# Kernel optimization log

Measured on AMD Instinct MI355X. Metric: run time of the kernel, lower is better.

Reference implementation:

```python
import jax, jax.numpy as jnp
import numpy as np

NEG = -1e10

def setup_inputs() -> dict:
    key = jax.random.key(0)
    ks = jax.random.split(key, 7)
    B, Q, K = 8, 128, 512
    d_q, d_kv, d_attn = 512, 512, 256
    query = jax.random.normal(ks[0], (B, Q, d_q), dtype=jnp.float32)
    kv = jax.random.normal(ks[1], (B, K, d_kv), dtype=jnp.float32)
    query_len = jax.random.randint(ks[2], (B,), 1, Q + 1)
    kv_len = jax.random.randint(ks[3], (B,), 1, K + 1)
    # h2attn: Linear(d_q+d_kv, d_attn) -> weight [d_attn, d_q+d_kv], bias [d_attn]
    W = jax.random.normal(ks[4], (d_attn, d_q + d_kv), dtype=jnp.float32) / np.sqrt(d_q + d_kv)
    b = jnp.zeros((d_attn,), dtype=jnp.float32)
    v = jax.random.normal(ks[5], (d_attn,), dtype=jnp.float32)
    return {"query": query, "kv": kv, "W": W, "b": b, "v": v,
            "query_len": query_len, "kv_len": kv_len}

def reference(query, kv, W, b, v, query_len, kv_len):
    B, Q, d_q = query.shape
    _, K, d_kv = kv.shape
    # Split the concat-linear: W @ [q; kv] == Wq @ q + Wk @ kv (same math, no huge concat)
    Wq, Wk = W[:, :d_q], W[:, d_q:]
    q_proj = jnp.einsum('bqd,ad->bqa', query, Wq)   # [B,Q,d_attn]
    k_proj = jnp.einsum('bkd,ad->bka', kv, Wk)      # [B,K,d_attn]
    e = jnp.tanh(q_proj[:, :, None, :] + k_proj[:, None, :, :] + b)  # [B,Q,K,d_attn]
    score = jnp.einsum('bqka,a->bqk', e, v)          # [B,Q,K]
    mask_q = jnp.arange(Q)[None, :] < query_len[:, None]   # [B,Q]
    mask_k = jnp.arange(K)[None, :] < kv_len[:, None]      # [B,K]
    score = jnp.where(mask_q[:, :, None], score, NEG)
    score = jnp.where(mask_k[:, None, :], score, NEG)
    attn = jax.nn.softmax(score, axis=-1)
    out = jnp.einsum('bqk,bkd->bqd', attn, kv)       # [B,Q,d_kv]
    return out
```

## Files before the change

kernel.cpp:

```cpp
#include <hip/hip_runtime.h>

#define NEGV (-10000000000.0f)

typedef unsigned short u16;
typedef _Float16 __attribute__((ext_vector_type(8))) f16x8;
typedef _Float16 __attribute__((ext_vector_type(4))) f16x4;
typedef __attribute__((ext_vector_type(4))) float f32x4;

__device__ __forceinline__ u16 f2fh(float f) {
  _Float16 h = (_Float16)f;
  return __builtin_bit_cast(u16, h);
}

__device__ __forceinline__ void gload16(const u16* g, u16* l) {
  __builtin_amdgcn_global_load_lds(
      (const __attribute__((address_space(1))) void*)g,
      (__attribute__((address_space(3))) void*)l, 16, 0, 0);
}

__device__ __forceinline__ f16x8 cvt8(float4 x, float4 y) {
  f16x8 o;
  o[0] = (_Float16)x.x; o[1] = (_Float16)x.y;
  o[2] = (_Float16)x.z; o[3] = (_Float16)x.w;
  o[4] = (_Float16)y.x; o[5] = (_Float16)y.y;
  o[6] = (_Float16)y.z; o[7] = (_Float16)y.w;
  return o;
}

__device__ __forceinline__ void mfma_tile(const u16* sA, const u16* sB,
                                          int l, int wr, int wc,
                                          f32x4 (*acc)[2]) {
#pragma unroll
  for (int ks = 0; ks < 2; ks++) {
    f16x8 af[2], bfr[2];
#pragma unroll
    for (int f = 0; f < 2; f++) {
      int cb = (ks * 32 + ((l >> 4) << 3)) << 1;
      int row = wr * 32 + f * 16 + (l & 15);
      af[f] = *(const f16x8*)((const char*)sA + row * 128 + (cb ^ ((row & 7) << 4)));
      int col = wc * 32 + f * 16 + (l & 15);
      bfr[f] = *(const f16x8*)((const char*)sB + col * 128 + (cb ^ ((col & 7) << 4)));
    }
#pragma unroll
    for (int fm = 0; fm < 2; fm++)
#pragma unroll
      for (int fn = 0; fn < 2; fn++)
        acc[fm][fn] = __builtin_amdgcn_mfma_f32_16x16x32_f16(
            af[fm], bfr[fn], acc[fm][fn], 0, 0, 0);
  }
}

__global__ __launch_bounds__(256) void proj_mfma(
    const float* __restrict__ query, const float* __restrict__ kv,
    const float* __restrict__ W, const float* __restrict__ bias,
    float* __restrict__ qpE, float* __restrict__ kpE)
{
  __shared__ __align__(16) u16 sA[8 * 512];
  __shared__ __align__(16) u16 sB[8 * 512];
  const int id = blockIdx.x, t = threadIdx.x;

  const float *A, *B; float* C;
  int lda, ldb, ldc, bm, bn;
  const float* bp = nullptr;
  if (id < 64) {
    A = query; lda = 512; B = W; ldb = 1024;
    C = qpE; ldc = 256;
    bm = (id >> 2) * 64; bn = (id & 3) * 64;
    bp = bias;
  } else {
    int r = id - 64;
    int b = r >> 5, w5 = r & 31;
    A = W + 512; lda = 1024;
    B = kv + (size_t)b * 512 * 512; ldb = 512;
    C = kpE + (size_t)b * 256 * 512; ldc = 512;
    bm = (w5 & 3) * 64; bn = (w5 >> 2) * 64;
  }

  const int l = t & 63, w = t >> 6;
  const int wr = w >> 1, wc = w & 1;
  const int r0 = t >> 3, oc = t & 7;
  const int sw0 = (oc * 16) ^ ((r0 & 7) << 4);

  f32x4 acc[2][2] = {};
  float4 a00, a01, a10, a11, b00, b01, b10, b11;

  auto LOAD = [&](int k0) {
    const float* pa0 = A + (size_t)(bm + r0) * lda + k0 + oc * 8;
    const float* pa1 = pa0 + (size_t)32 * lda;
    a00 = *(const float4*)pa0; a01 = *(const float4*)(pa0 + 4);
    a10 = *(const float4*)pa1; a11 = *(const float4*)(pa1 + 4);
    const float* pb0 = B + (size_t)(bn + r0) * ldb + k0 + oc * 8;
    const float* pb1 = pb0 + (size_t)32 * ldb;
    b00 = *(const float4*)pb0; b01 = *(const float4*)(pb0 + 4);
    b10 = *(const float4*)pb1; b11 = *(const float4*)(pb1 + 4);
  };
  auto WRITE = [&]() {
    *(f16x8*)((char*)sA + r0 * 128 + sw0)        = cvt8(a00, a01);
    *(f16x8*)((char*)sA + (r0 + 32) * 128 + sw0) = cvt8(a10, a11);
    *(f16x8*)((char*)sB + r0 * 128 + sw0)        = cvt8(b00, b01);
    *(f16x8*)((char*)sB + (r0 + 32) * 128 + sw0) = cvt8(b10, b11);
  };

  LOAD(0);
  for (int k0 = 0; k0 < 512; k0 += 64) {
    __syncthreads();
    WRITE();
    if (k0 + 64 < 512) LOAD(k0 + 64);
    __syncthreads();
    mfma_tile(sA, sB, l, wr, wc, acc);
  }

#pragma unroll
  for (int fm = 0; fm < 2; fm++)
#pragma unroll
    for (int fn = 0; fn < 2; fn++) {
      int cn = bn + wc * 32 + fn * 16 + (l & 15);
      float bv = bp ? bp[cn] : 0.0f;
#pragma unroll
      for (int j = 0; j < 4; j++) {
        int rm = bm + wr * 32 + fm * 16 + (l >> 4) * 4 + j;
        C[(size_t)rm * ldc + cn] = __expf((acc[fm][fn][j] + bv) * 2.0f);
      }
    }
}

__global__ __launch_bounds__(256) void score_softmax(
    const float* __restrict__ qpE,
    const float* __restrict__ kpE,
    const float* __restrict__ v,
    const int* __restrict__ qlen_p, const int* __restrict__ klen_p,
    u16* __restrict__ P)
{
  const int b = blockIdx.y, q0 = blockIdx.x * 2, t = threadIdx.x;
  const int qlen = qlen_p[b], klen = klen_p[b];
  const int w = t >> 6, l = t & 63;
  const int k1 = w * 64 + l, k2 = k1 + 256;
  u16* Pb = P + (size_t)(b * 128 + q0) * 512;

  if (q0 >= qlen) {
    const u16 uh = f2fh(1.0f / 512.0f);
    Pb[k1] = uh; Pb[k2] = uh;
    Pb[512 + k1] = uh; Pb[512 + k2] = uh;
    return;
  }

  __shared__ float sEq[512];
  __shared__ float sV2[256];
  __shared__ float sRed[16];

  sV2[t] = 2.0f * v[t];
  sEq[t]       = qpE[(size_t)(b * 128 + q0) * 256 + t];
  sEq[256 + t] = qpE[(size_t)(b * 128 + q0 + 1) * 256 + t];
  __syncthreads();

  const float* kc = kpE + (size_t)b * 256 * 512;
  float s1a = 0.f, s2a = 0.f, s1b = 0.f, s2b = 0.f;

  if (w * 64 < klen) {
    if (256 + w * 64 < klen) {
#pragma unroll 8
      for (int a = 0; a < 256; a++) {
        float ek1 = kc[(size_t)a * 512 + k1];
        float ek2 = kc[(size_t)a * 512 + k2];
        float vv = sV2[a];
        float eqA = sEq[a], eqB = sEq[256 + a];
        s1a = fmaf(-vv, __builtin_amdgcn_rcpf(fmaf(eqA, ek1, 1.0f)), s1a);
        s2a = fmaf(-vv, __builtin_amdgcn_rcpf(fmaf(eqA, ek2, 1.0f)), s2a);
        s1b = fmaf(-vv, __builtin_amdgcn_rcpf(fmaf(eqB, ek1, 1.0f)), s1b);
        s2b = fmaf(-vv, __builtin_amdgcn_rcpf(fmaf(eqB, ek2, 1.0f)), s2b);
      }
    } else {
#pragma unroll 8
      for (int a = 0; a < 256; a++) {
        float ek1 = kc[(size_t)a * 512 + k1];
        float vv = sV2[a];
        float eqA = sEq[a], eqB = sEq[256 + a];
        s1a = fmaf(-vv, __builtin_amdgcn_rcpf(fmaf(eqA, ek1, 1.0f)), s1a);
        s1b = fmaf(-vv, __builtin_amdgcn_rcpf(fmaf(eqB, ek1, 1.0f)), s1b);
      }
    }
  }

  if (k1 >= klen) { s1a = NEGV; s1b = NEGV; }
  if (k2 >= klen) { s2a = NEGV; s2b = NEGV; }

  float mA = fmaxf(s1a, s2a), mB = fmaxf(s1b, s2b);
#pragma unroll
  for (int off = 32; off > 0; off >>= 1) {
    mA = fmaxf(mA, __shfl_xor(mA, off));
    mB = fmaxf(mB, __shfl_xor(mB, off));
  }
  if (l == 0) { sRed[w * 4 + 0] = mA; sRed[w * 4 + 1] = mB; }
  __syncthreads();
  const float MA = fmaxf(fmaxf(sRed[0], sRed[4]), fmaxf(sRed[8],  sRed[12]));
  const float MB = fmaxf(fmaxf(sRed[1], sRed[5]), fmaxf(sRed[9],  sRed[13]));

  float e1a = __expf(s1a - MA), e2a = __expf(s2a - MA);
  float e1b = __expf(s1b - MB), e2b = __expf(s2b - MB);
  float suA = e1a + e2a, suB = e1b + e2b;
#pragma unroll
  for (int off = 32; off > 0; off >>= 1) {
    suA += __shfl_xor(suA, off);
    suB += __shfl_xor(suB, off);
  }
  if (l == 0) { sRed[w * 4 + 2] = suA; sRed[w * 4 + 3] = suB; }
  __syncthreads();
  const float SA = (sRed[2] + sRed[6]) + (sRed[10] + sRed[14]);
  const float SB = (sRed[3] + sRed[7]) + (sRed[11] + sRed[15]);
  const float rA = __fdividef(1.0f, SA);
  const float rB = __fdividef(1.0f, SB);

  Pb[k1] = f2fh(e1a * rA);
  Pb[k2] = f2fh(e2a * rA);
  if (q0 + 1 < qlen) {
    Pb[512 + k1] = f2fh(e1b * rB);
    Pb[512 + k2] = f2fh(e2b * rB);
  } else {
    const u16 uh = f2fh(1.0f / 512.0f);
    Pb[512 + k1] = uh;
    Pb[512 + k2] = uh;
  }
}

__global__ __launch_bounds__(256) void pv_mfma(
    const u16* __restrict__ P, const float* __restrict__ kv,
    float* __restrict__ out)
{
  __shared__ __align__(16) u16 sA[8 * 512];
  __shared__ __align__(16) u16 sB[8 * 512];
  const int id = blockIdx.x, t = threadIdx.x;
  const int b = id >> 4, r = id & 15;
  const int bm = (r >> 3) * 64, bn = (r & 7) * 64;

  const u16* Ab = P + (size_t)b * 128 * 512;
  const float* Bb = kv + (size_t)b * 512 * 512;

  const int l = t & 63, w = t >> 6;
  const int wr = w >> 1, wc = w & 1;
  const int srow = l >> 3, scol = ((l & 7) ^ srow) << 3;

  const int dq = t & 15, kq = t >> 4;

  float4 v0, v1, v2, v3;
  auto LOADB = [&](int k0) {
    const float* p = Bb + (size_t)(k0 + kq * 4) * 512 + bn + dq * 4;
    v0 = *(const float4*)p;
    v1 = *(const float4*)(p + 512);
    v2 = *(const float4*)(p + 1024);
    v3 = *(const float4*)(p + 1536);
  };
  auto WRITEB = [&]() {
#define WRB(jj, ee)                                                       \
    { int d = dq * 4 + jj;                                                \
      f16x4 c; c[0] = (_Float16)v0.ee; c[1] = (_Float16)v1.ee;            \
      c[2] = (_Float16)v2.ee; c[3] = (_Float16)v3.ee;                     \
      *(f16x4*)((char*)sB + d * 128 +                                     \
                ((((kq >> 1) * 16) ^ ((d & 7) << 4)) + (kq & 1) * 8)) = c; }
    WRB(0, x) WRB(1, y) WRB(2, z) WRB(3, w)
#undef WRB
  };

  f32x4 acc[2][2] = {};
  LOADB(0);
  for (int k0 = 0; k0 < 512; k0 += 64) {
    __syncthreads();
    WRITEB();
#pragma unroll
    for (int i = 0; i < 2; i++) {
      int s = w * 2 + i;
      gload16(Ab + (size_t)(bm + s * 8 + srow) * 512 + k0 + scol, sA + s * 512);
    }
    if (k0 + 64 < 512) LOADB(k0 + 64);
    __syncthreads();
    mfma_tile(sA, sB, l, wr, wc, acc);
  }

  float* Cb = out + (size_t)b * 128 * 512;
#pragma unroll
  for (int fm = 0; fm < 2; fm++)
#pragma unroll
    for (int fn = 0; fn < 2; fn++) {
      int cn = bn + wc * 32 + fn * 16 + (l & 15);
#pragma unroll
      for (int j = 0; j < 4; j++) {
        int rm = bm + wr * 32 + fm * 16 + (l >> 4) * 4 + j;
        Cb[(size_t)rm * 512 + cn] = acc[fm][fn][j];
      }
    }
}

extern "C" void kernel_launch(void* const* d_in, const int* in_sizes, int n_in,
                              void* d_out, int out_size, void* d_ws, size_t ws_size,
                              hipStream_t stream)
{
  const float* query = (const float*)d_in[0];
  const float* kv    = (const float*)d_in[1];
  const float* W     = (const float*)d_in[2];
  const float* bbias = (const float*)d_in[3];
  const float* v     = (const float*)d_in[4];
  const int*   qlen  = (const int*)d_in[5];
  const int*   klen  = (const int*)d_in[6];
  float* out = (float*)d_out;

  float* qpE = (float*)d_ws;
  float* kpE = qpE + 1024 * 256;
  u16*   P   = (u16*)(kpE + 8 * 256 * 512);

  proj_mfma<<<dim3(320), 256, 0, stream>>>(query, kv, W, bbias, qpE, kpE);

  score_softmax<<<dim3(64, 8), 256, 0, stream>>>(
      qpE, kpE, v, qlen, klen, P);

  pv_mfma<<<dim3(128), 256, 0, stream>>>(P, kv, out);
}
```

Baseline: 44.65 us.

## Fuse score softmax with PV product and precompute kv column sums

Merges the score/softmax kernel and the MFMA PV kernel into one kernel. Each block handles four queries, keeps the probabilities in LDS, and does P·V with FP32 FMAs over only the valid keys (up to klen), so the fp16 P round-trip through global memory and one launch go away. Fully masked query rows now take the mean of kv, computed once by extra column-sum blocks in the projection kernel using atomics, with a memset added to zero that buffer. The cost is that PV now runs on scalar FP32 instead of matrix cores, and the block is larger and uses a lot of LDS, which may limit occupancy.

```diff
diff --git a/kernel.cpp b/kernel.cpp
--- a/kernel.cpp
+++ b/kernel.cpp
@@ -4,19 +4,7 @@
 
 typedef unsigned short u16;
 typedef _Float16 __attribute__((ext_vector_type(8))) f16x8;
-typedef _Float16 __attribute__((ext_vector_type(4))) f16x4;
 typedef __attribute__((ext_vector_type(4))) float f32x4;
-
-__device__ __forceinline__ u16 f2fh(float f) {
-  _Float16 h = (_Float16)f;
-  return __builtin_bit_cast(u16, h);
-}
-
-__device__ __forceinline__ void gload16(const u16* g, u16* l) {
-  __builtin_amdgcn_global_load_lds(
-      (const __attribute__((address_space(1))) void*)g,
-      (__attribute__((address_space(3))) void*)l, 16, 0, 0);
-}
 
 __device__ __forceinline__ f16x8 cvt8(float4 x, float4 y) {
   f16x8 o;
@@ -50,14 +38,31 @@
   }
 }
 
-__global__ __launch_bounds__(256) void proj_mfma(
+__global__ __launch_bounds__(256) void proj_colsum(
     const float* __restrict__ query, const float* __restrict__ kv,
     const float* __restrict__ W, const float* __restrict__ bias,
-    float* __restrict__ qpE, float* __restrict__ kpE)
+    float* __restrict__ qpE, float* __restrict__ kpE,
+    float* __restrict__ kvsum)
 {
+  const int id = blockIdx.x, t = threadIdx.x;
+
+  if (id >= 320) {
+    const int cb = id - 320;
+    const int b = cb >> 3, kt = cb & 7;
+    const float* p = kv + ((size_t)b * 512 + kt * 64) * 512 + 2 * t;
+    float s0 = 0.f, s1 = 0.f;
+#pragma unroll 8
+    for (int kk = 0; kk < 64; kk++) {
+      float2 x = *(const float2*)(p + (size_t)kk * 512);
+      s0 += x.x; s1 += x.y;
+    }
+    atomicAdd(&kvsum[b * 512 + 2 * t], s0);
+    atomicAdd(&kvsum[b * 512 + 2 * t + 1], s1);
+    return;
+  }
+
   __shared__ __align__(16) u16 sA[8 * 512];
   __shared__ __align__(16) u16 sB[8 * 512];
-  const int id = blockIdx.x, t = threadIdx.x;
 
   const float *A, *B; float* C;
   int lda, ldb, ldc, bm, bn;
@@ -124,169 +129,141 @@
     }
 }
 
-__global__ __launch_bounds__(256) void score_softmax(
+__global__ __launch_bounds__(512) void score_pv(
     const float* __restrict__ qpE,
     const float* __restrict__ kpE,
     const float* __restrict__ v,
     const int* __restrict__ qlen_p, const int* __restrict__ klen_p,
-    u16* __restrict__ P)
-{
-  const int b = blockIdx.y, q0 = blockIdx.x * 2, t = threadIdx.x;
-  const int qlen = qlen_p[b], klen = klen_p[b];
-  const int w = t >> 6, l = t & 63;
-  const int k1 = w * 64 + l, k2 = k1 + 256;
-  u16* Pb = P + (size_t)(b * 128 + q0) * 512;
-
-  if (q0 >= qlen) {
-    const u16 uh = f2fh(1.0f / 512.0f);
-    Pb[k1] = uh; Pb[k2] = uh;
-    Pb[512 + k1] = uh; Pb[512 + k2] = uh;
-    return;
-  }
-
-  __shared__ float sEq[512];
-  __shared__ float sV2[256];
-  __shared__ float sRed[16];
-
-  sV2[t] = 2.0f * v[t];
-  sEq[t]       = qpE[(size_t)(b * 128 + q0) * 256 + t];
-  sEq[256 + t] = qpE[(size_t)(b * 128 + q0 + 1) * 256 + t];
-  __syncthreads();
-
-  const float* kc = kpE + (size_t)b * 256 * 512;
-  float s1a = 0.f, s2a = 0.f, s1b = 0.f, s2b = 0.f;
-
-  if (w * 64 < klen) {
-    if (256 + w * 64 < klen) {
-#pragma unroll 8
-      for (int a = 0; a < 256; a++) {
-        float ek1 = kc[(size_t)a * 512 + k1];
-        float ek2 = kc[(size_t)a * 512 + k2];
-        float vv = sV2[a];
-        float eqA = sEq[a], eqB = sEq[256 + a];
-        s1a = fmaf(-vv, __builtin_amdgcn_rcpf(fmaf(eqA, ek1, 1.0f)), s1a);
-        s2a = fmaf(-vv, __builtin_amdgcn_rcpf(fmaf(eqA, ek2, 1.0f)), s2a);
-        s1b = fmaf(-vv, __builtin_amdgcn_rcpf(fmaf(eqB, ek1, 1.0f)), s1b);
-        s2b = fmaf(-vv, __builtin_amdgcn_rcpf(fmaf(eqB, ek2, 1.0f)), s2b);
-      }
-    } else {
-#pragma unroll 8
-      for (int a = 0; a < 256; a++) {
-        float ek1 = kc[(size_t)a * 512 + k1];
-        float vv = sV2[a];
-        float eqA = sEq[a], eqB = sEq[256 + a];
-        s1a = fmaf(-vv, __builtin_amdgcn_rcpf(fmaf(eqA, ek1, 1.0f)), s1a);
-        s1b = fmaf(-vv, __builtin_amdgcn_rcpf(fmaf(eqB, ek1, 1.0f)), s1b);
-      }
-    }
-  }
-
-  if (k1 >= klen) { s1a = NEGV; s1b = NEGV; }
-  if (k2 >= klen) { s2a = NEGV; s2b = NEGV; }
-
-  float mA = fmaxf(s1a, s2a), mB = fmaxf(s1b, s2b);
-#pragma unroll
-  for (int off = 32; off > 0; off >>= 1) {
-    mA = fmaxf(mA, __shfl_xor(mA, off));
-    mB = fmaxf(mB, __shfl_xor(mB, off));
-  }
-  if (l == 0) { sRed[w * 4 + 0] = mA; sRed[w * 4 + 1] = mB; }
-  __syncthreads();
-  const float MA = fmaxf(fmaxf(sRed[0], sRed[4]), fmaxf(sRed[8],  sRed[12]));
-  const float MB = fmaxf(fmaxf(sRed[1], sRed[5]), fmaxf(sRed[9],  sRed[13]));
-
-  float e1a = __expf(s1a - MA), e2a = __expf(s2a - MA);
-  float e1b = __expf(s1b - MB), e2b = __expf(s2b - MB);
-  float suA = e1a + e2a, suB = e1b + e2b;
-#pragma unroll
-  for (int off = 32; off > 0; off >>= 1) {
-    suA += __shfl_xor(suA, off);
-    suB += __shfl_xor(suB, off);
-  }
-  if (l == 0) { sRed[w * 4 + 2] = suA; sRed[w * 4 + 3] = suB; }
-  __syncthreads();
-  const float SA = (sRed[2] + sRed[6]) + (sRed[10] + sRed[14]);
-  const float SB = (sRed[3] + sRed[7]) + (sRed[11] + sRed[15]);
-  const float rA = __fdividef(1.0f, SA);
-  const float rB = __fdividef(1.0f, SB);
-
-  Pb[k1] = f2fh(e1a * rA);
-  Pb[k2] = f2fh(e2a * rA);
-  if (q0 + 1 < qlen) {
-    Pb[512 + k1] = f2fh(e1b * rB);
-    Pb[512 + k2] = f2fh(e2b * rB);
-  } else {
-    const u16 uh = f2fh(1.0f / 512.0f);
-    Pb[512 + k1] = uh;
-    Pb[512 + k2] = uh;
-  }
-}
-
-__global__ __launch_bounds__(256) void pv_mfma(
-    const u16* __restrict__ P, const float* __restrict__ kv,
+    const float* __restrict__ kv,
+    const float* __restrict__ kvsum,
     float* __restrict__ out)
 {
-  __shared__ __align__(16) u16 sA[8 * 512];
-  __shared__ __align__(16) u16 sB[8 * 512];
-  const int id = blockIdx.x, t = threadIdx.x;
-  const int b = id >> 4, r = id & 15;
-  const int bm = (r >> 3) * 64, bn = (r & 7) * 64;
-
-  const u16* Ab = P + (size_t)b * 128 * 512;
-  const float* Bb = kv + (size_t)b * 512 * 512;
-
-  const int l = t & 63, w = t >> 6;
-  const int wr = w >> 1, wc = w & 1;
-  const int srow = l >> 3, scol = ((l & 7) ^ srow) << 3;
-
-  const int dq = t & 15, kq = t >> 4;
-
-  float4 v0, v1, v2, v3;
-  auto LOADB = [&](int k0) {
-    const float* p = Bb + (size_t)(k0 + kq * 4) * 512 + bn + dq * 4;
-    v0 = *(const float4*)p;
-    v1 = *(const float4*)(p + 512);
-    v2 = *(const float4*)(p + 1024);
-    v3 = *(const float4*)(p + 1536);
-  };
-  auto WRITEB = [&]() {
-#define WRB(jj, ee)                                                       \
-    { int d = dq * 4 + jj;                                                \
-      f16x4 c; c[0] = (_Float16)v0.ee; c[1] = (_Float16)v1.ee;            \
-      c[2] = (_Float16)v2.ee; c[3] = (_Float16)v3.ee;                     \
-      *(f16x4*)((char*)sB + d * 128 +                                     \
-                ((((kq >> 1) * 16) ^ ((d & 7) << 4)) + (kq & 1) * 8)) = c; }
-    WRB(0, x) WRB(1, y) WRB(2, z) WRB(3, w)
-#undef WRB
-  };
-
-  f32x4 acc[2][2] = {};
-  LOADB(0);
-  for (int k0 = 0; k0 < 512; k0 += 64) {
-    __syncthreads();
-    WRITEB();
-#pragma unroll
-    for (int i = 0; i < 2; i++) {
-      int s = w * 2 + i;
-      gload16(Ab + (size_t)(bm + s * 8 + srow) * 512 + k0 + scol, sA + s * 512);
-    }
-    if (k0 + 64 < 512) LOADB(k0 + 64);
-    __syncthreads();
-    mfma_tile(sA, sB, l, wr, wc, acc);
-  }
-
-  float* Cb = out + (size_t)b * 128 * 512;
-#pragma unroll
-  for (int fm = 0; fm < 2; fm++)
-#pragma unroll
-    for (int fn = 0; fn < 2; fn++) {
-      int cn = bn + wc * 32 + fn * 16 + (l & 15);
+  const int b = blockIdx.y, q0 = blockIdx.x * 4, t = threadIdx.x;
+  const int qlen = qlen_p[b], klen = klen_p[b];
+  float* outb = out + (size_t)(b * 128 + q0) * 512;
+
+  if (q0 >= qlen) {
+    float m = kvsum[b * 512 + t] * (1.0f / 512.0f);
+#pragma unroll
+    for (int r = 0; r < 4; r++) outb[(size_t)r * 512 + t] = m;
+    return;
+  }
+
+  __shared__ float sW[512][4];
+  __shared__ float sEq[256][4];
+  __shared__ float sV2[256];
+  __shared__ float sRed[8][8];
+  __shared__ float sAcc[4][4 * 512];
+
+  {
+    int a = t & 255, rr = t >> 8;
+    sEq[a][rr]     = qpE[(size_t)(b * 128 + q0 + rr) * 256 + a];
+    sEq[a][rr + 2] = qpE[(size_t)(b * 128 + q0 + rr + 2) * 256 + a];
+    if (t < 256) sV2[t] = 2.0f * v[t];
+  }
+  __syncthreads();
+
+  const int w = t >> 6, l = t & 63;
+  const int k = t;
+
+  float s[4] = {0.f, 0.f, 0.f, 0.f};
+  if (w * 64 < klen) {
+    const float* kc = kpE + (size_t)b * 256 * 512 + k;
+#pragma unroll 8
+    for (int a = 0; a < 256; a++) {
+      float ek = kc[(size_t)a * 512];
+      f32x4 eq = *(const f32x4*)&sEq[a][0];
+      float vv = sV2[a];
+#pragma unroll
+      for (int r = 0; r < 4; r++)
+        s[r] = fmaf(-vv, __builtin_amdgcn_rcpf(fmaf(eq[r], ek, 1.0f)), s[r]);
+    }
+  }
+  if (k >= klen) {
+#pragma unroll
+    for (int r = 0; r < 4; r++) s[r] = NEGV;
+  }
+
+#pragma unroll
+  for (int r = 0; r < 4; r++) {
+    float x = s[r];
+#pragma unroll
+    for (int off = 32; off > 0; off >>= 1) x = fmaxf(x, __shfl_xor(x, off));
+    if (l == 0) sRed[w][r] = x;
+  }
+  __syncthreads();
+  float e[4];
+#pragma unroll
+  for (int r = 0; r < 4; r++) {
+    float mm = sRed[0][r];
+#pragma unroll
+    for (int i = 1; i < 8; i++) mm = fmaxf(mm, sRed[i][r]);
+    e[r] = __expf(s[r] - mm);
+  }
+  __syncthreads();
+#pragma unroll
+  for (int r = 0; r < 4; r++) {
+    float x = e[r];
+#pragma unroll
+    for (int off = 32; off > 0; off >>= 1) x += __shfl_xor(x, off);
+    if (l == 0) sRed[w][4 + r] = x;
+  }
+  __syncthreads();
+  f32x4 p;
+#pragma unroll
+  for (int r = 0; r < 4; r++) {
+    float S = 0.f;
+#pragma unroll
+    for (int i = 0; i < 8; i++) S += sRed[i][4 + r];
+    p[r] = e[r] * __fdividef(1.0f, S);
+  }
+  *(f32x4*)&sW[k][0] = p;
+  __syncthreads();
+
+  f32x4 accA[4] = {}, accB[4] = {};
+  const int kb = w * 64;
+  const int ke = (kb + 64 < klen) ? kb + 64 : klen;
+  const float* kvb = kv + (size_t)b * 512 * 512 + l;
+#pragma unroll 4
+  for (int kk = kb; kk < ke; kk++) {
+    f32x4 p4 = *(const f32x4*)&sW[kk][0];
+    const float* row = kvb + (size_t)kk * 512;
+    float x[8];
+#pragma unroll
+    for (int j = 0; j < 8; j++) x[j] = row[j * 64];
+#pragma unroll
+    for (int r = 0; r < 4; r++)
 #pragma unroll
       for (int j = 0; j < 4; j++) {
-        int rm = bm + wr * 32 + fm * 16 + (l >> 4) * 4 + j;
-        Cb[(size_t)rm * 512 + cn] = acc[fm][fn][j];
+        accA[r][j] = fmaf(p4[r], x[j],     accA[r][j]);
+        accB[r][j] = fmaf(p4[r], x[4 + j], accB[r][j]);
       }
-    }
+  }
+
+  if (w < 4) {
+#pragma unroll
+    for (int r = 0; r < 4; r++)
+#pragma unroll
+      for (int j = 0; j < 8; j++)
+        sAcc[w][r * 512 + l + j * 64] = (j < 4) ? accA[r][j] : accB[r][j - 4];
+  }
+  __syncthreads();
+  if (w >= 4) {
+#pragma unroll
+    for (int r = 0; r < 4; r++)
+#pragma unroll
+      for (int j = 0; j < 8; j++)
+        sAcc[w - 4][r * 512 + l + j * 64] += (j < 4) ? accA[r][j] : accB[r][j - 4];
+  }
+  __syncthreads();
+
+#pragma unroll
+  for (int r = 0; r < 4; r++) {
+    float val = (sAcc[0][r * 512 + t] + sAcc[1][r * 512 + t]) +
+                (sAcc[2][r * 512 + t] + sAcc[3][r * 512 + t]);
+    if (q0 + r >= qlen) val = kvsum[b * 512 + t] * (1.0f / 512.0f);
+    outb[(size_t)r * 512 + t] = val;
+  }
 }
 
 extern "C" void kernel_launch(void* const* d_in, const int* in_sizes, int n_in,
@@ -302,14 +279,15 @@
   const int*   klen  = (const int*)d_in[6];
   float* out = (float*)d_out;
 
-  float* qpE = (float*)d_ws;
-  float* kpE = qpE + 1024 * 256;
-  u16*   P   = (u16*)(kpE + 8 * 256 * 512);
-
-  proj_mfma<<<dim3(320), 256, 0, stream>>>(query, kv, W, bbias, qpE, kpE);
-
-  score_softmax<<<dim3(64, 8), 256, 0, stream>>>(
-      qpE, kpE, v, qlen, klen, P);
-
-  pv_mfma<<<dim3(128), 256, 0, stream>>>(P, kv, out);
-}
+  float* qpE   = (float*)d_ws;
+  float* kpE   = qpE + 1024 * 256;
+  float* kvsum = kpE + 8 * 256 * 512;
+
+  hipMemsetAsync(kvsum, 0, 8 * 512 * sizeof(float), stream);
+
+  proj_colsum<<<dim3(384), 256, 0, stream>>>(
+      query, kv, W, bbias, qpE, kpE, kvsum);
+
+  score_pv<<<dim3(32, 8), 512, 0, stream>>>(
+      qpE, kpE, v, qlen, klen, kv, kvsum, out);
+}
```

After: 54.43 us. +21.9%, slower.
